# Optimization experiments

Measured on AMD Instinct MI355X. Metric: run time of the kernel, lower is better.

The kernel has to match this reference:

```python
import math
import jax, jax.numpy as jnp
import numpy as np

B, T, D = 4, 2048, 768
NH, DH = 12, 64

def setup_inputs() -> dict:
    key = jax.random.key(0)
    k1, k2, k3 = jax.random.split(key, 3)
    scale_attn = 1.0 / math.sqrt(D)
    scale_proj = 1.0 / math.sqrt(D)
    return {
        "x": jax.random.normal(k1, (B, T, D), dtype=jnp.float32),
        "w_attn": jax.random.normal(k2, (D, 3 * D), dtype=jnp.float32) * scale_attn,
        "b_attn": jnp.zeros((3 * D,), dtype=jnp.float32),
        "w_proj": jax.random.normal(k3, (D, D), dtype=jnp.float32) * scale_proj,
        "b_proj": jnp.zeros((D,), dtype=jnp.float32),
    }

def reference(x, w_attn, b_attn, w_proj, b_proj):
    Bx, Tx, Dx = x.shape
    qkv = x @ w_attn + b_attn                     # [B, T, 3D]
    q, k, v = jnp.split(qkv, 3, axis=-1)          # each [B, T, D]
    # [B, T, D] -> [B, NH, T, DH]
    def to_heads(t):
        return t.reshape(Bx, Tx, NH, DH).transpose(0, 2, 1, 3)
    q, k, v = to_heads(q), to_heads(k), to_heads(v)
    attn = jnp.einsum("bhqd,bhkd->bhqk", q, k) / math.sqrt(DH)
    causal = jnp.tril(jnp.ones((Tx, Tx), dtype=bool))
    attn = jnp.where(causal[None, None, :, :], attn, -jnp.inf)
    attn = jax.nn.softmax(attn, axis=-1)
    out = jnp.einsum("bhqk,bhkd->bhqd", attn, v)  # [B, NH, T, DH]
    out = out.transpose(0, 2, 1, 3).reshape(Bx, Tx, Dx)
    out = out @ w_proj + b_proj
    return (out, (k, v))
```

## Files before the change

### kernel.cpp

```cpp
#include <hip/hip_runtime.h>
#include <hip/hip_bf16.h>

typedef unsigned short ushort_t;
typedef __attribute__((ext_vector_type(8))) short short8;
typedef __attribute__((ext_vector_type(4))) float f32x4;

#define B_    4
#define T_    2048
#define D_    768
#define NH_   12
#define DH_   64
#define KDIM  768

__device__ __forceinline__ ushort_t f2bf(float f) {
  union { float f; unsigned u; } c; c.f = f;
  unsigned u = c.u;
  return (ushort_t)((u + 0x7FFFu + ((u >> 16) & 1u)) >> 16);
}

__device__ __forceinline__ unsigned cvt_pk_bf16(float lo, float hi) {
  unsigned r;
  asm("v_cvt_pk_bf16_f32 %0, %1, %2" : "=v"(r) : "v"(lo), "v"(hi));
  return r;
}

__device__ __forceinline__ void gload_lds16(const void* g, void* l) {
  __builtin_amdgcn_global_load_lds(
      (const __attribute__((address_space(1))) unsigned int*)g,
      (__attribute__((address_space(3))) unsigned int*)l, 16, 0, 0);
}

__global__ void cvt_bf16_vec(const float* __restrict__ in,
                             ushort_t* __restrict__ out, int n4) {
  int i = blockIdx.x * blockDim.x + threadIdx.x;
  if (i >= n4) return;
  float4 v = ((const float4*)in)[i];
  ushort4 o;
  o.x = f2bf(v.x); o.y = f2bf(v.y); o.z = f2bf(v.z); o.w = f2bf(v.w);
  ((ushort4*)out)[i] = o;
}

__global__ void transpose_cvt(const float* __restrict__ in,
                              ushort_t* __restrict__ out, int R, int C) {
  __shared__ float tile[32][33];
  int c0 = blockIdx.x * 32, r0 = blockIdx.y * 32;
  int tx = threadIdx.x, ty = threadIdx.y;
#pragma unroll
  for (int j = 0; j < 32; j += 8)
    tile[ty + j][tx] = in[(size_t)(r0 + ty + j) * C + c0 + tx];
  __syncthreads();
#pragma unroll
  for (int j = 0; j < 32; j += 8)
    out[(size_t)(c0 + ty + j) * R + r0 + tx] = f2bf(tile[tx][ty + j]);
}

__device__ __forceinline__ void gemm128_mainloop(
    const ushort_t* __restrict__ A, const ushort_t* __restrict__ BT,
    int m0, int n0, ushort_t* lds, f32x4 acc[4][4]) {
  const int t = threadIdx.x;
  const int l = t & 63;
  const int w = t >> 6;
  const int wm = w >> 1, wn = w & 1;
  const int c0 = t, c1 = t + 256;
  const ushort_t* ga0 = A + (size_t)(m0 + (c0 >> 2)) * KDIM + ((c0 & 3) << 3);
  const ushort_t* ga1 = A + (size_t)(m0 + (c1 >> 2)) * KDIM + ((c1 & 3) << 3);
  const ushort_t* gb0 = BT + (size_t)(n0 + (c0 >> 2)) * KDIM + ((c0 & 3) << 3);
  const ushort_t* gb1 = BT + (size_t)(n0 + (c1 >> 2)) * KDIM + ((c1 & 3) << 3);
  ushort_t* la0 = lds + (0 * 256 + w * 64) * 8;
  ushort_t* la1 = lds + (1 * 256 + w * 64) * 8;
  ushort_t* lb0 = lds + 4096 + (0 * 256 + w * 64) * 8;
  ushort_t* lb1 = lds + 4096 + (1 * 256 + w * 64) * 8;
  const int frag_off = ((l & 15) * 32) + ((l >> 4) * 8);

  for (int k0 = 0; k0 < KDIM; k0 += 32) {
    gload_lds16(ga0 + k0, la0);
    gload_lds16(ga1 + k0, la1);
    gload_lds16(gb0 + k0, lb0);
    gload_lds16(gb1 + k0, lb1);
    __syncthreads();
    short8 af[4], bfv[4];
#pragma unroll
    for (int mt = 0; mt < 4; ++mt)
      af[mt] = *(const short8*)&lds[(wm * 64 + mt * 16) * 32 + frag_off];
#pragma unroll
    for (int nt = 0; nt < 4; ++nt)
      bfv[nt] = *(const short8*)&lds[4096 + (wn * 64 + nt * 16) * 32 + frag_off];
#pragma unroll
    for (int mt = 0; mt < 4; ++mt)
#pragma unroll
      for (int nt = 0; nt < 4; ++nt)
        acc[mt][nt] = __builtin_amdgcn_mfma_f32_16x16x32_bf16(
            af[mt], bfv[nt], acc[mt][nt], 0, 0, 0);
    __syncthreads();
  }
}

__global__ __launch_bounds__(256) void gemm_qkv_kernel(
    const ushort_t* __restrict__ xbf, const ushort_t* __restrict__ wT,
    const float* __restrict__ bias, ushort_t* __restrict__ qbf,
    float* __restrict__ kout, float* __restrict__ vout,
    ushort_t* __restrict__ kbf, ushort_t* __restrict__ vtbf) {
  __shared__ ushort_t lds[8192];
  int bid = blockIdx.x;
  int m0 = (bid & 63) << 7;
  int n0 = (bid >> 6) << 7;
  f32x4 acc[4][4];
  f32x4 zero = {0.f, 0.f, 0.f, 0.f};
#pragma unroll
  for (int a = 0; a < 4; ++a)
#pragma unroll
    for (int b = 0; b < 4; ++b) acc[a][b] = zero;
  gemm128_mainloop(xbf, wT, m0, n0, lds, acc);

  const float QSC = 0.125f * 1.44269504089f;
  const int l = threadIdx.x & 63, w = threadIdx.x >> 6;
  const int wm = w >> 1, wn = w & 1;
  const int sec = n0 / 768;
  const int b = m0 >> 11;
  const int tt_base = (m0 & 2047) + wm * 64;
#pragma unroll
  for (int nt = 0; nt < 4; ++nt) {
    int n = n0 + wn * 64 + nt * 16 + (l & 15);
    float bv = bias[n];
    int nn = n - sec * 768;
    int h = nn >> 6, dh = nn & 63;
    size_t head_base = ((size_t)(b * NH_ + h) * T_);
#pragma unroll
    for (int mt = 0; mt < 4; ++mt) {
      int tt0 = tt_base + mt * 16 + ((l >> 4) << 2);
      float vals[4];
#pragma unroll
      for (int r = 0; r < 4; ++r) vals[r] = acc[mt][nt][r] + bv;
      if (sec == 0) {
#pragma unroll
        for (int r = 0; r < 4; ++r)
          qbf[((head_base + tt0 + r) << 6) + dh] = f2bf(vals[r] * QSC);
      } else if (sec == 1) {
#pragma unroll
        for (int r = 0; r < 4; ++r) {
          size_t idx = ((head_base + tt0 + r) << 6) + dh;
          kout[idx] = vals[r];
          kbf[idx] = f2bf(vals[r]);
        }
      } else {
#pragma unroll
        for (int r = 0; r < 4; ++r)
          vout[((head_base + tt0 + r) << 6) + dh] = vals[r];
        ushort4 pk;
        pk.x = f2bf(vals[0]); pk.y = f2bf(vals[1]);
        pk.z = f2bf(vals[2]); pk.w = f2bf(vals[3]);
        *(ushort4*)&vtbf[((size_t)(b * NH_ + h) * DH_ + dh) * T_ + tt0] = pk;
      }
    }
  }
}

__global__ __launch_bounds__(256) void gemm_proj_kernel(
    const ushort_t* __restrict__ abf, const ushort_t* __restrict__ wT,
    const float* __restrict__ bias, float* __restrict__ out) {
  __shared__ ushort_t lds[8192];
  int bid = blockIdx.x;
  int m0 = (bid & 63) << 7;
  int n0 = (bid >> 6) << 7;
  f32x4 acc[4][4];
  f32x4 zero = {0.f, 0.f, 0.f, 0.f};
#pragma unroll
  for (int a = 0; a < 4; ++a)
#pragma unroll
    for (int b = 0; b < 4; ++b) acc[a][b] = zero;
  gemm128_mainloop(abf, wT, m0, n0, lds, acc);

  const int l = threadIdx.x & 63, w = threadIdx.x >> 6;
  const int wm = w >> 1, wn = w & 1;
#pragma unroll
  for (int nt = 0; nt < 4; ++nt) {
    int n = n0 + wn * 64 + nt * 16 + (l & 15);
    float bv = bias[n];
#pragma unroll
    for (int mt = 0; mt < 4; ++mt) {
#pragma unroll
      for (int r = 0; r < 4; ++r) {
        int m = m0 + wm * 64 + mt * 16 + ((l >> 4) << 2) + r;
        out[(size_t)m * D_ + n] = acc[mt][nt][r] + bv;
      }
    }
  }
}

__device__ __forceinline__ void strip_exp_store(
    f32x4 s4[4], int gq, bool diag, int kvb, int g, int qi, char* pbase) {
  if (diag) {
#pragma unroll
    for (int nt = 0; nt < 4; ++nt)
#pragma unroll
      for (int r = 0; r < 4; ++r) {
        int gk = kvb + nt * 16 + g * 4 + r;
        if (gk > gq) s4[nt][r] = -1e30f;
      }
  }
#pragma unroll
  for (int nt = 0; nt < 4; ++nt) {
    float p0 = exp2f(s4[nt][0]);
    float p1 = exp2f(s4[nt][1]);
    float p2 = exp2f(s4[nt][2]);
    float p3 = exp2f(s4[nt][3]);
    uint2 pk;
    pk.x = cvt_pk_bf16(p0, p1);
    pk.y = cvt_pk_bf16(p2, p3);
    *(uint2*)(pbase + ((nt * 32 + g * 8) ^ ((qi & 7) << 4))) = pk;
  }
}

__global__ __launch_bounds__(256, 4) void attn_fwd_kernel(
    const ushort_t* __restrict__ qbf, const ushort_t* __restrict__ kbf,
    const ushort_t* __restrict__ vtbf, ushort_t* __restrict__ obf) {
  __shared__ ushort_t Kl[2][4096];
  __shared__ ushort_t Vt[2][4096];
  __shared__ ushort_t Pl[4][1024];
  const int bid = blockIdx.x;
  const int swz = (bid & 7) * 96 + (bid >> 3);
  const int jp = swz & 15;
  const int bh = swz >> 4;
  const int qlo = jp << 6, qhi = (31 - jp) << 6;
  const int lastH = 31 - jp, lastL = jp;
  const int t = threadIdx.x, l = t & 63, w = t >> 6;
  const int g = l >> 4, qi = l & 15;

  const ushort_t* Qb = qbf + (size_t)bh * T_ * DH_;
  const ushort_t* Kb = kbf + (size_t)bh * T_ * DH_;
  const ushort_t* Vb = vtbf + (size_t)bh * DH_ * T_;

  const int row0 = t >> 3, ch0 = t & 7, row1 = row0 + 32;
  const ushort_t* gK0 = Kb + row0 * DH_ + ((ch0 ^ (row0 & 7)) << 3);
  const ushort_t* gK1 = Kb + row1 * DH_ + ((ch0 ^ (row1 & 7)) << 3);
  const ushort_t* gV0 = Vb + (size_t)row0 * T_ + ((ch0 ^ (row0 & 7)) << 3);
  const ushort_t* gV1 = Vb + (size_t)row1 * T_ + ((ch0 ^ (row1 & 7)) << 3);

  short8 aqH[2], aqL[2];
  {
    const int qrH = qhi + w * 16 + qi, qrL = qlo + w * 16 + qi;
    aqH[0] = *(const short8*)&Qb[(size_t)qrH * DH_ + (g << 3)];
    aqH[1] = *(const short8*)&Qb[(size_t)qrH * DH_ + (g << 3) + 32];
    aqL[0] = *(const short8*)&Qb[(size_t)qrL * DH_ + (g << 3)];
    aqL[1] = *(const short8*)&Qb[(size_t)qrL * DH_ + (g << 3) + 32];
  }

  short8 ones;
#pragma unroll
  for (int j = 0; j < 8; ++j) ones[j] = (short)0x3F80;

  f32x4 oH[4], oL[4], alH, alL;
  f32x4 zero = {0.f, 0.f, 0.f, 0.f};
#pragma unroll
  for (int nt = 0; nt < 4; ++nt) { oH[nt] = zero; oL[nt] = zero; }
  alH = zero; alL = zero;

  gload_lds16(gK0, &Kl[0][w * 512]);
  gload_lds16(gK1, &Kl[0][2048 + w * 512]);
  gload_lds16(gV0, &Vt[0][w * 512]);
  gload_lds16(gV1, &Vt[0][2048 + w * 512]);

  char* pb = (char*)&Pl[w][0] + qi * 128;

  for (int kt = 0; kt <= lastH; ++kt) {
    const int buf = kt & 1;
    const int kvb = kt << 6;
    asm volatile("s_waitcnt vmcnt(0)" ::: "memory");
    __builtin_amdgcn_sched_barrier(0);
    __builtin_amdgcn_s_barrier();
    __builtin_amdgcn_sched_barrier(0);
    if (kt < lastH) {
      const int nx = kt + 1;
      gload_lds16(gK0 + (size_t)nx * 4096, &Kl[buf ^ 1][w * 512]);
      gload_lds16(gK1 + (size_t)nx * 4096, &Kl[buf ^ 1][2048 + w * 512]);
      gload_lds16(gV0 + (size_t)nx * 64, &Vt[buf ^ 1][w * 512]);
      gload_lds16(gV1 + (size_t)nx * 64, &Vt[buf ^ 1][2048 + w * 512]);
    }
    const bool loAct = (kt <= lastL);

    f32x4 s4H[4], s4L[4];
#pragma unroll
    for (int nt = 0; nt < 4; ++nt) { s4H[nt] = zero; s4L[nt] = zero; }
#pragma unroll
    for (int h2 = 0; h2 < 2; ++h2) {
      short8 bk[4];
#pragma unroll
      for (int nt = 0; nt < 4; ++nt)
        bk[nt] = *(const short8*)&Kl[buf][((nt * 16 + qi) << 6) +
                                          (((g + 4 * h2) ^ (qi & 7)) << 3)];
#pragma unroll
      for (int nt = 0; nt < 4; ++nt)
        s4H[nt] = __builtin_amdgcn_mfma_f32_16x16x32_bf16(bk[nt], aqH[h2],
                                                          s4H[nt], 0, 0, 0);
      if (loAct) {
#pragma unroll
        for (int nt = 0; nt < 4; ++nt)
          s4L[nt] = __builtin_amdgcn_mfma_f32_16x16x32_bf16(bk[nt], aqL[h2],
                                                            s4L[nt], 0, 0, 0);
      }
    }

    strip_exp_store(s4H, qhi + w * 16 + qi, kt == lastH, kvb, g, qi, pb);
#pragma unroll
    for (int k2 = 0; k2 < 2; ++k2) {
      short8 av[4];
#pragma unroll
      for (int nt = 0; nt < 4; ++nt)
        av[nt] = *(const short8*)&Vt[buf][((nt * 16 + qi) << 6) +
                                          (((g + 4 * k2) ^ (qi & 7)) << 3)];
      short8 pf = *(const short8*)(pb + ((g * 16 + k2 * 64) ^ ((qi & 7) << 4)));
#pragma unroll
      for (int nt = 0; nt < 4; ++nt)
        oH[nt] = __builtin_amdgcn_mfma_f32_16x16x32_bf16(av[nt], pf, oH[nt],
                                                         0, 0, 0);
      alH = __builtin_amdgcn_mfma_f32_16x16x32_bf16(ones, pf, alH, 0, 0, 0);
    }

    if (loAct) {
      strip_exp_store(s4L, qlo + w * 16 + qi, kt == lastL, kvb, g, qi, pb);
#pragma unroll
      for (int k2 = 0; k2 < 2; ++k2) {
        short8 av[4];
#pragma unroll
        for (int nt = 0; nt < 4; ++nt)
          av[nt] = *(const short8*)&Vt[buf][((nt * 16 + qi) << 6) +
                                            (((g + 4 * k2) ^ (qi & 7)) << 3)];
        short8 pf = *(const short8*)(pb + ((g * 16 + k2 * 64) ^ ((qi & 7) << 4)));
#pragma unroll
        for (int nt = 0; nt < 4; ++nt)
          oL[nt] = __builtin_amdgcn_mfma_f32_16x16x32_bf16(av[nt], pf, oL[nt],
                                                           0, 0, 0);
        alL = __builtin_amdgcn_mfma_f32_16x16x32_bf16(ones, pf, alL, 0, 0, 0);
      }
    }
  }

  const int b = bh / NH_, h = bh - b * NH_;
#pragma unroll
  for (int s = 0; s < 2; ++s) {
    f32x4* o = s ? oL : oH;
    float inv = 1.f / (s ? alL[0] : alH[0]);
    int qs = (s ? qlo : qhi) + w * 16 + qi;
    size_t rowb = (size_t)(b * T_ + qs) * D_ + h * DH_;
#pragma unroll
    for (int nt = 0; nt < 4; ++nt) {
      ushort4 pk;
      pk.x = f2bf(o[nt][0] * inv);
      pk.y = f2bf(o[nt][1] * inv);
      pk.z = f2bf(o[nt][2] * inv);
      pk.w = f2bf(o[nt][3] * inv);
      *(ushort4*)&obf[rowb + nt * 16 + g * 4] = pk;
    }
  }
}

extern "C" void kernel_launch(void* const* d_in, const int* in_sizes, int n_in,
                              void* d_out, int out_size, void* d_ws, size_t ws_size,
                              hipStream_t stream) {
  const float* x      = (const float*)d_in[0];
  const float* w_attn = (const float*)d_in[1];
  const float* b_attn = (const float*)d_in[2];
  const float* w_proj = (const float*)d_in[3];
  const float* b_proj = (const float*)d_in[4];

  float* out  = (float*)d_out;
  float* kout = out + (size_t)B_ * T_ * D_;
  float* vout = kout + (size_t)B_ * T_ * D_;

  char* ws = (char*)d_ws;
  ushort_t* xbf = (ushort_t*)(ws);
  ushort_t* wTa = (ushort_t*)(ws + 12582912);
  ushort_t* wTp = (ushort_t*)(ws + 16121856);
  ushort_t* qbf = (ushort_t*)(ws + 17301504);
  ushort_t* kbf = (ushort_t*)(ws + 29884416);
  ushort_t* vtbf = (ushort_t*)(ws + 42467328);
  ushort_t* abf = xbf;

  cvt_bf16_vec<<<6144, 256, 0, stream>>>(x, xbf, (B_ * T_ * D_) / 4);
  dim3 tb(32, 8);
  transpose_cvt<<<dim3(72, 24), tb, 0, stream>>>(w_attn, wTa, D_, 3 * D_);
  transpose_cvt<<<dim3(24, 24), tb, 0, stream>>>(w_proj, wTp, D_, D_);

  gemm_qkv_kernel<<<64 * 18, 256, 0, stream>>>(xbf, wTa, b_attn, qbf, kout, vout,
                                               kbf, vtbf);
  attn_fwd_kernel<<<48 * 16, 256, 0, stream>>>(qbf, kbf, vtbf, abf);
  gemm_proj_kernel<<<64 * 6, 256, 0, stream>>>(abf, wTp, b_proj, out);
}
```

Baseline: 147.0 us.

## Split high and low query strips across separate waves in attention blocks

The attention block grows from 4 to 8 waves. Each wave now owns one 16-row query strip, either from the high tile or the low tile, where before each wave processed both strips. Per-wave registers fall and more waves are available to hide latency, and K/V tile loads are spread over twice as many threads. The cost is that the low-tile waves go idle once their causal range ends while still joining the block barriers, so load across waves is unbalanced. The extra P buffers also raise LDS use per block.

After: 140.1 us. -4.7%, faster.

```diff
diff --git a/kernel.cpp b/kernel.cpp
--- a/kernel.cpp
+++ b/kernel.cpp
@@ -211,12 +211,12 @@
   }
 }
 
-__global__ __launch_bounds__(256, 4) void attn_fwd_kernel(
+__global__ __launch_bounds__(512, 6) void attn_fwd_kernel(
     const ushort_t* __restrict__ qbf, const ushort_t* __restrict__ kbf,
     const ushort_t* __restrict__ vtbf, ushort_t* __restrict__ obf) {
   __shared__ ushort_t Kl[2][4096];
   __shared__ ushort_t Vt[2][4096];
-  __shared__ ushort_t Pl[4][1024];
+  __shared__ ushort_t Pl[8][1024];
   const int bid = blockIdx.x;
   const int swz = (bid & 7) * 96 + (bid >> 3);
   const int jp = swz & 15;
@@ -225,40 +225,38 @@
   const int lastH = 31 - jp, lastL = jp;
   const int t = threadIdx.x, l = t & 63, w = t >> 6;
   const int g = l >> 4, qi = l & 15;
+  const bool isHi = (w < 4);
+  const int wc = isHi ? w : (w - 4);
+  const int qs0 = (isHi ? qhi : qlo) + wc * 16;
+  const int lastMe = isHi ? lastH : lastL;
 
   const ushort_t* Qb = qbf + (size_t)bh * T_ * DH_;
   const ushort_t* Kb = kbf + (size_t)bh * T_ * DH_;
   const ushort_t* Vb = vtbf + (size_t)bh * DH_ * T_;
 
-  const int row0 = t >> 3, ch0 = t & 7, row1 = row0 + 32;
+  const int row0 = t >> 3, ch0 = t & 7;
   const ushort_t* gK0 = Kb + row0 * DH_ + ((ch0 ^ (row0 & 7)) << 3);
-  const ushort_t* gK1 = Kb + row1 * DH_ + ((ch0 ^ (row1 & 7)) << 3);
   const ushort_t* gV0 = Vb + (size_t)row0 * T_ + ((ch0 ^ (row0 & 7)) << 3);
-  const ushort_t* gV1 = Vb + (size_t)row1 * T_ + ((ch0 ^ (row1 & 7)) << 3);
-
-  short8 aqH[2], aqL[2];
+
+  short8 aq[2];
   {
-    const int qrH = qhi + w * 16 + qi, qrL = qlo + w * 16 + qi;
-    aqH[0] = *(const short8*)&Qb[(size_t)qrH * DH_ + (g << 3)];
-    aqH[1] = *(const short8*)&Qb[(size_t)qrH * DH_ + (g << 3) + 32];
-    aqL[0] = *(const short8*)&Qb[(size_t)qrL * DH_ + (g << 3)];
-    aqL[1] = *(const short8*)&Qb[(size_t)qrL * DH_ + (g << 3) + 32];
+    const int qr = qs0 + qi;
+    aq[0] = *(const short8*)&Qb[(size_t)qr * DH_ + (g << 3)];
+    aq[1] = *(const short8*)&Qb[(size_t)qr * DH_ + (g << 3) + 32];
   }
 
   short8 ones;
 #pragma unroll
   for (int j = 0; j < 8; ++j) ones[j] = (short)0x3F80;
 
-  f32x4 oH[4], oL[4], alH, alL;
+  f32x4 o[4], al;
   f32x4 zero = {0.f, 0.f, 0.f, 0.f};
 #pragma unroll
-  for (int nt = 0; nt < 4; ++nt) { oH[nt] = zero; oL[nt] = zero; }
-  alH = zero; alL = zero;
+  for (int nt = 0; nt < 4; ++nt) o[nt] = zero;
+  al = zero;
 
   gload_lds16(gK0, &Kl[0][w * 512]);
-  gload_lds16(gK1, &Kl[0][2048 + w * 512]);
   gload_lds16(gV0, &Vt[0][w * 512]);
-  gload_lds16(gV1, &Vt[0][2048 + w * 512]);
 
   char* pb = (char*)&Pl[w][0] + qi * 128;
 
@@ -272,76 +270,43 @@
     if (kt < lastH) {
       const int nx = kt + 1;
       gload_lds16(gK0 + (size_t)nx * 4096, &Kl[buf ^ 1][w * 512]);
-      gload_lds16(gK1 + (size_t)nx * 4096, &Kl[buf ^ 1][2048 + w * 512]);
       gload_lds16(gV0 + (size_t)nx * 64, &Vt[buf ^ 1][w * 512]);
-      gload_lds16(gV1 + (size_t)nx * 64, &Vt[buf ^ 1][2048 + w * 512]);
-    }
-    const bool loAct = (kt <= lastL);
-
-    f32x4 s4H[4], s4L[4];
-#pragma unroll
-    for (int nt = 0; nt < 4; ++nt) { s4H[nt] = zero; s4L[nt] = zero; }
-#pragma unroll
-    for (int h2 = 0; h2 < 2; ++h2) {
-      short8 bk[4];
-#pragma unroll
-      for (int nt = 0; nt < 4; ++nt)
-        bk[nt] = *(const short8*)&Kl[buf][((nt * 16 + qi) << 6) +
-                                          (((g + 4 * h2) ^ (qi & 7)) << 3)];
-#pragma unroll
-      for (int nt = 0; nt < 4; ++nt)
-        s4H[nt] = __builtin_amdgcn_mfma_f32_16x16x32_bf16(bk[nt], aqH[h2],
-                                                          s4H[nt], 0, 0, 0);
-      if (loAct) {
-#pragma unroll
-        for (int nt = 0; nt < 4; ++nt)
-          s4L[nt] = __builtin_amdgcn_mfma_f32_16x16x32_bf16(bk[nt], aqL[h2],
-                                                            s4L[nt], 0, 0, 0);
-      }
-    }
-
-    strip_exp_store(s4H, qhi + w * 16 + qi, kt == lastH, kvb, g, qi, pb);
-#pragma unroll
-    for (int k2 = 0; k2 < 2; ++k2) {
-      short8 av[4];
-#pragma unroll
-      for (int nt = 0; nt < 4; ++nt)
-        av[nt] = *(const short8*)&Vt[buf][((nt * 16 + qi) << 6) +
-                                          (((g + 4 * k2) ^ (qi & 7)) << 3)];
-      short8 pf = *(const short8*)(pb + ((g * 16 + k2 * 64) ^ ((qi & 7) << 4)));
-#pragma unroll
-      for (int nt = 0; nt < 4; ++nt)
-        oH[nt] = __builtin_amdgcn_mfma_f32_16x16x32_bf16(av[nt], pf, oH[nt],
-                                                         0, 0, 0);
-      alH = __builtin_amdgcn_mfma_f32_16x16x32_bf16(ones, pf, alH, 0, 0, 0);
-    }
-
-    if (loAct) {
-      strip_exp_store(s4L, qlo + w * 16 + qi, kt == lastL, kvb, g, qi, pb);
+    }
+    if (kt <= lastMe) {
+      f32x4 s4[4];
+#pragma unroll
+      for (int nt = 0; nt < 4; ++nt) s4[nt] = zero;
+#pragma unroll
+      for (int h2 = 0; h2 < 2; ++h2) {
+#pragma unroll
+        for (int nt = 0; nt < 4; ++nt) {
+          short8 bk = *(const short8*)&Kl[buf][((nt * 16 + qi) << 6) +
+                                              (((g + 4 * h2) ^ (qi & 7)) << 3)];
+          s4[nt] = __builtin_amdgcn_mfma_f32_16x16x32_bf16(bk, aq[h2],
+                                                           s4[nt], 0, 0, 0);
+        }
+      }
+      strip_exp_store(s4, qs0 + qi, kt == lastMe, kvb, g, qi, pb);
 #pragma unroll
       for (int k2 = 0; k2 < 2; ++k2) {
-        short8 av[4];
-#pragma unroll
-        for (int nt = 0; nt < 4; ++nt)
-          av[nt] = *(const short8*)&Vt[buf][((nt * 16 + qi) << 6) +
-                                            (((g + 4 * k2) ^ (qi & 7)) << 3)];
         short8 pf = *(const short8*)(pb + ((g * 16 + k2 * 64) ^ ((qi & 7) << 4)));
 #pragma unroll
-        for (int nt = 0; nt < 4; ++nt)
-          oL[nt] = __builtin_amdgcn_mfma_f32_16x16x32_bf16(av[nt], pf, oL[nt],
-                                                           0, 0, 0);
-        alL = __builtin_amdgcn_mfma_f32_16x16x32_bf16(ones, pf, alL, 0, 0, 0);
+        for (int nt = 0; nt < 4; ++nt) {
+          short8 av = *(const short8*)&Vt[buf][((nt * 16 + qi) << 6) +
+                                               (((g + 4 * k2) ^ (qi & 7)) << 3)];
+          o[nt] = __builtin_amdgcn_mfma_f32_16x16x32_bf16(av, pf, o[nt],
+                                                          0, 0, 0);
+        }
+        al = __builtin_amdgcn_mfma_f32_16x16x32_bf16(ones, pf, al, 0, 0, 0);
       }
     }
   }
 
   const int b = bh / NH_, h = bh - b * NH_;
-#pragma unroll
-  for (int s = 0; s < 2; ++s) {
-    f32x4* o = s ? oL : oH;
-    float inv = 1.f / (s ? alL[0] : alH[0]);
-    int qs = (s ? qlo : qhi) + w * 16 + qi;
-    size_t rowb = (size_t)(b * T_ + qs) * D_ + h * DH_;
+  {
+    float inv = 1.f / al[0];
+    int q = qs0 + qi;
+    size_t rowb = (size_t)(b * T_ + q) * D_ + h * DH_;
 #pragma unroll
     for (int nt = 0; nt < 4; ++nt) {
       ushort4 pk;
@@ -383,6 +348,6 @@
 
   gemm_qkv_kernel<<<64 * 18, 256, 0, stream>>>(xbf, wTa, b_attn, qbf, kout, vout,
                                                kbf, vtbf);
-  attn_fwd_kernel<<<48 * 16, 256, 0, stream>>>(qbf, kbf, vtbf, abf);
+  attn_fwd_kernel<<<768, 512, 0, stream>>>(qbf, kbf, vtbf, abf);
   gemm_proj_kernel<<<64 * 6, 256, 0, stream>>>(abf, wTp, b_proj, out);
 }
```
